# Kernel tuning notes

Measured on AMD Instinct MI355X. Metric: run time of the kernel, lower is better.

## Reference

```python
import jax, jax.numpy as jnp
import numpy as np
from jax.scipy.special import logsumexp

NUM_STATES = 16
NUM_CHAINS = 8
NUM_NODES = 1500
NUM_ITERS = 500


def setup_inputs() -> dict:
    key = jax.random.key(0)
    k1, k2, k3, k4 = jax.random.split(key, 4)
    return {
        "unnormalized_state_init": jax.random.normal(k1, (NUM_STATES, NUM_CHAINS), jnp.float32),
        "unnormalized_chain_weights": jax.random.normal(k2, (NUM_ITERS, NUM_CHAINS), jnp.float32),
        "unnormalized_emission_matrix": jax.random.normal(k3, (NUM_STATES, 1, NUM_NODES), jnp.float32),
        "unnormalized_transition_matrix": jax.random.normal(k4, (NUM_CHAINS, NUM_STATES, NUM_STATES), jnp.float32),
    }


def reference(unnormalized_state_init, unnormalized_chain_weights,
              unnormalized_emission_matrix, unnormalized_transition_matrix):
    # log_transform_params: normalize each distribution in log domain
    log_state_init = jax.nn.log_softmax(unnormalized_state_init, axis=0)          # (S,C): over states
    log_chain_weights = jax.nn.log_softmax(unnormalized_chain_weights, axis=-1)   # (T,C): over chains
    log_emission = jax.nn.log_softmax(unnormalized_emission_matrix, axis=-1)      # (S,1,N): over nodes
    log_T_ = jax.nn.log_softmax(unnormalized_transition_matrix, axis=-1)          # (C,S,S): over next state

    T = unnormalized_chain_weights.shape[0]

    # chain-marginalized transition matrix (computed as in torch forward_model; not used downstream)
    log_mean_cw = logsumexp(log_chain_weights, axis=0) - jnp.log(jnp.asarray(T, log_chain_weights.dtype))
    _log_transition_matrix = logsumexp(log_T_ + log_mean_cw[:, None, None], axis=0)

    # sequential HMM prior recursion over tiny (S,C) state via scan
    def step(h, _):
        # h: (S,C) -> h.T: (C,S); logsumexp over previous-state axis
        new = logsumexp(h.T[:, :, None] + log_T_, axis=1).T  # (S,C)
        return new, new

    h0 = log_state_init
    _, hs = jax.lax.scan(step, h0, None, length=T - 1)
    log_hidden_state_probs = jnp.concatenate([h0[None], hs], axis=0)  # (T,S,C)

    # emission broadcast: (S,1,N) + (T,S,C,1) -> (T,S,C,N), then add chain weights
    log_observed_state_probs_ = (log_emission[None]
                                 + log_hidden_state_probs[..., None]
                                 + log_chain_weights[:, None, :, None])
    # marginalize over states then chains
    log_observed_state_probs = logsumexp(log_observed_state_probs_, axis=(1, 2))  # (T,N)
    return (log_observed_state_probs, log_observed_state_probs_, log_hidden_state_probs)
```

## Files before the change

kernel.cpp:

```cpp
#include <hip/hip_runtime.h>
#include <hip/hip_bf16.h>

#define S 16
#define C 8
#define SC 128
#define TT 500
#define NN 1500
#define NF4 375
#define CHUNK 25
#define NCHUNK 20

__device__ __forceinline__ float fexp2(float x) { return exp2f(x); }
__device__ __forceinline__ float flog2(float x) { return log2f(x); }

#define L2E 1.4426950408889634f
#define LN2 0.6931471805599453f

typedef float f4v __attribute__((ext_vector_type(4)));

#define MM(dst, Asrc, Bsrc) do {                                          \
    __syncthreads();                                                      \
    {   const int c_ = tid >> 5; const int e0_ = tid & 31;                \
        for (int r_ = 0; r_ < 8; ++r_) {                                  \
            const int e_ = e0_ + (r_ << 5);                               \
            const int i_ = e_ >> 4; const int l_ = e_ & 15;               \
            float acc_ = 0.f;                                             \
            _Pragma("unroll")                                             \
            for (int s_ = 0; s_ < S; ++s_)                                \
                acc_ += Asrc[(c_ * S + i_) * S + s_] *                    \
                        Bsrc[(c_ * S + s_) * S + l_];                     \
            dst[(c_ * S + i_) * S + l_] = acc_;                          \
        } }                                                               \
} while (0)

__global__ __launch_bounds__(256) void hmm_setup(
    const float* __restrict__ usi,
    const float* __restrict__ ucw,
    const float* __restrict__ uem,
    const float* __restrict__ utm,
    float* __restrict__ ws_lcw,
    float* __restrict__ ws_pT,
    float* __restrict__ ws_q,
    float* __restrict__ ws_emlse)
{
    __shared__ float bufT[C * S * S];
    __shared__ float bufX[C * S * S];
    __shared__ float bufY[C * S * S];
    __shared__ float bufZ[C * S * S];
    __shared__ float qbuf[C * S];
    const int tid = threadIdx.x;

    for (int t = tid; t < TT; t += 256) {
        float x[C]; float m = -1e30f;
#pragma unroll
        for (int cc = 0; cc < C; ++cc) { x[cc] = ucw[t * C + cc]; m = fmaxf(m, x[cc]); }
        float acc = 0.f;
#pragma unroll
        for (int cc = 0; cc < C; ++cc) acc += fexp2((x[cc] - m) * L2E);
        const float lse = m + flog2(acc) * LN2;
#pragma unroll
        for (int cc = 0; cc < C; ++cc) ws_lcw[t * C + cc] = x[cc] - lse;
    }

    {
        const int row = tid >> 4;
        const int ln  = tid & 15;
        const float* rp = uem + row * NN;
        float a = 0.f;
        for (int n = ln; n < NN; n += 16) a += fexp2(rp[n] * L2E);
#pragma unroll
        for (int off = 8; off >= 1; off >>= 1) a += __shfl_xor(a, off);
        if (ln == 0) ws_emlse[row] = flog2(a) * LN2;
    }

    if (tid < SC) {
        float x[S]; float m = -1e30f;
#pragma unroll
        for (int k = 0; k < S; ++k) { x[k] = utm[tid * S + k]; m = fmaxf(m, x[k]); }
        float acc = 0.f; float e[S];
#pragma unroll
        for (int k = 0; k < S; ++k) { e[k] = fexp2((x[k] - m) * L2E); acc += e[k]; }
        const float inv = 1.f / acc;
#pragma unroll
        for (int k = 0; k < S; ++k) {
            const float v = e[k] * inv;
            bufT[tid * S + k] = v;
            ws_pT[tid * S + k] = v;
        }
    }

    if (tid < C) {
        const int cc = tid;
        float x[S]; float m = -1e30f;
#pragma unroll
        for (int s0 = 0; s0 < S; ++s0) { x[s0] = usi[s0 * C + cc]; m = fmaxf(m, x[s0]); }
        float acc = 0.f; float e[S];
#pragma unroll
        for (int s0 = 0; s0 < S; ++s0) { e[s0] = fexp2((x[s0] - m) * L2E); acc += e[s0]; }
        const float inv = 1.f / acc;
#pragma unroll
        for (int s0 = 0; s0 < S; ++s0) {
            const float v = e[s0] * inv;
            qbuf[cc * S + s0] = v;
            ws_q[cc * S + s0] = v;
        }
    }

    MM(bufX, bufT, bufT);
    MM(bufY, bufX, bufX);
    MM(bufZ, bufY, bufY);
    MM(bufX, bufZ, bufZ);
    MM(bufY, bufX, bufZ);
    MM(bufX, bufY, bufT);
    __syncthreads();

    const int c5 = tid >> 4;
    const int l5 = tid & 15;
    float Acol[S];
    if (tid < 128) {
#pragma unroll
        for (int s0 = 0; s0 < S; ++s0) Acol[s0] = bufX[(c5 * S + s0) * S + l5];
    }
    for (int k = 1; k < NCHUNK; ++k) {
        float acc = 0.f;
        if (tid < 128) {
#pragma unroll
            for (int s0 = 0; s0 < S; ++s0) acc += qbuf[c5 * S + s0] * Acol[s0];
        }
        __syncthreads();
        if (tid < 128) {
            qbuf[c5 * S + l5] = acc;
            ws_q[k * SC + c5 * S + l5] = acc;
        }
        __syncthreads();
    }
}

__global__ __launch_bounds__(512) void fused_bcast(
    const float* __restrict__ uem,
    const float* __restrict__ ws_lcw,
    const float* __restrict__ ws_pT,
    const float* __restrict__ ws_q,
    const float* __restrict__ ws_emlse,
    float* __restrict__ out1,
    float* __restrict__ out2,
    float* __restrict__ out3)
{
    const int t = blockIdx.x;
    const int tid = threadIdx.x;
    __shared__ float hc[SC];
    __shared__ float Ws[S];
    __shared__ float em[S];

    if (tid >= 64 && tid < 64 + S) em[tid - 64] = ws_emlse[tid - 64];

    if (tid < 64) {
        const int c = tid >> 3;
        const int j = tid & 7;
        float Ta[S], Tb[S];
#pragma unroll
        for (int s0 = 0; s0 < S; ++s0) {
            Ta[s0] = ws_pT[(c * S + s0) * S + j];
            Tb[s0] = ws_pT[(c * S + s0) * S + j + 8];
        }
        const int k = t / CHUNK;
        const int m = t - k * CHUNK;
        float pa = ws_q[k * SC + c * S + j];
        float pb = ws_q[k * SC + c * S + j + 8];
        const int base = c << 3;
        for (int i = 0; i < m; ++i) {
            float pv[S];
#pragma unroll
            for (int q = 0; q < 8; ++q) {
                pv[q]     = __shfl(pa, base + q);
                pv[q + 8] = __shfl(pb, base + q);
            }
            float a0 = 0.f, a1 = 0.f, a2 = 0.f, a3 = 0.f;
            float b0 = 0.f, b1 = 0.f, b2 = 0.f, b3 = 0.f;
#pragma unroll
            for (int s0 = 0; s0 < S; s0 += 4) {
                a0 = fmaf(pv[s0],     Ta[s0],     a0);
                a1 = fmaf(pv[s0 + 1], Ta[s0 + 1], a1);
                a2 = fmaf(pv[s0 + 2], Ta[s0 + 2], a2);
                a3 = fmaf(pv[s0 + 3], Ta[s0 + 3], a3);
                b0 = fmaf(pv[s0],     Tb[s0],     b0);
                b1 = fmaf(pv[s0 + 1], Tb[s0 + 1], b1);
                b2 = fmaf(pv[s0 + 2], Tb[s0 + 2], b2);
                b3 = fmaf(pv[s0 + 3], Tb[s0 + 3], b3);
            }
            pa = (a0 + a1) + (a2 + a3);
            pb = (b0 + b1) + (b2 + b3);
        }
        const float la = flog2(pa) * LN2;
        const float lb = flog2(pb) * LN2;
        out3[(size_t)t * SC + j * C + c]       = la;
        out3[(size_t)t * SC + (j + 8) * C + c] = lb;
        const float w = ws_lcw[t * C + c];
        hc[j * C + c]       = la + w;
        hc[(j + 8) * C + c] = lb + w;
    }
    __syncthreads();
    if (tid < S) {
        float mx = -1e30f;
#pragma unroll
        for (int cc = 0; cc < C; ++cc) mx = fmaxf(mx, hc[tid * C + cc]);
        float acc = 0.f;
#pragma unroll
        for (int cc = 0; cc < C; ++cc) acc += fexp2((hc[tid * C + cc] - mx) * L2E);
        Ws[tid] = mx + flog2(acc) * LN2;
    }
    __syncthreads();

    if (tid < NF4) {
        f4v acc1 = {0.f, 0.f, 0.f, 0.f};
        float* o2t = out2 + (size_t)t * SC * NN + tid * 4;
        for (int s0 = 0; s0 < S; ++s0) {
            f4v e = *(const f4v*)(uem + s0 * NN + tid * 4);
            const float el = em[s0];
            e -= el;
            const float w = Ws[s0];
            acc1.x += fexp2((e.x + w) * L2E);
            acc1.y += fexp2((e.y + w) * L2E);
            acc1.z += fexp2((e.z + w) * L2E);
            acc1.w += fexp2((e.w + w) * L2E);
            float* orow = o2t + (size_t)s0 * C * NN;
#pragma unroll
            for (int cc = 0; cc < C; ++cc) {
                const float hv = hc[s0 * C + cc];
                f4v v = e + hv;
                __builtin_nontemporal_store(v, (f4v*)(orow + (size_t)cc * NN));
            }
        }
        f4v r;
        r.x = flog2(acc1.x) * LN2;
        r.y = flog2(acc1.y) * LN2;
        r.z = flog2(acc1.z) * LN2;
        r.w = flog2(acc1.w) * LN2;
        *(f4v*)(out1 + (size_t)t * NN + tid * 4) = r;
    }
}

extern "C" void kernel_launch(void* const* d_in, const int* in_sizes, int n_in,
                              void* d_out, int out_size, void* d_ws, size_t ws_size,
                              hipStream_t stream)
{
    const float* usi = (const float*)d_in[0];
    const float* ucw = (const float*)d_in[1];
    const float* uem = (const float*)d_in[2];
    const float* utm = (const float*)d_in[3];

    float* out  = (float*)d_out;
    float* out1 = out;
    float* out2 = out + 750000;
    float* out3 = out + 750000 + 96000000;

    float* ws       = (float*)d_ws;
    float* ws_lcw   = ws;
    float* ws_pT    = ws + 4000;
    float* ws_q     = ws + 6048;
    float* ws_emlse = ws + 8608;

    hmm_setup<<<1, 256, 0, stream>>>(usi, ucw, uem, utm, ws_lcw, ws_pT, ws_q, ws_emlse);
    fused_bcast<<<TT, 512, 0, stream>>>(uem, ws_lcw, ws_pT, ws_q, ws_emlse,
                                        out1, out2, out3);
}
```

Baseline: 139.6 us.

## Move HMM recursion into single setup block and split broadcast into separate kernels

The hidden-state recursion moves out of every broadcast block and into one 1024-thread setup kernel, where 16 wavefronts each run a 32-step chunk from precomputed T^32 powers. That kernel also writes out3 and a per-(t,s) chain-weighted log term. The old fused broadcast kernel is split into an out1 kernel, which computes the reduction in the probability domain as exp(em)*g, and a streaming out2 kernel over a (16,500) grid that uses regular instead of nontemporal stores. This removes the redundant per-block sequential recursion (up to 24 steps per block) and gives the big store more, smaller blocks. The cost is an extra launch, a serial single-block setup phase, and a second read of uem.

New measurement: 172.5 us. 1.24x slower.

```diff
diff --git a/kernel.cpp b/kernel.cpp
--- a/kernel.cpp
+++ b/kernel.cpp
@@ -7,8 +7,8 @@
 #define TT 500
 #define NN 1500
 #define NF4 375
-#define CHUNK 25
-#define NCHUNK 20
+#define CHUNK 32
+#define NCHUNK 16
 
 __device__ __forceinline__ float fexp2(float x) { return exp2f(x); }
 __device__ __forceinline__ float flog2(float x) { return log2f(x); }
@@ -20,37 +20,40 @@
 
 #define MM(dst, Asrc, Bsrc) do {                                          \
     __syncthreads();                                                      \
-    {   const int c_ = tid >> 5; const int e0_ = tid & 31;                \
-        for (int r_ = 0; r_ < 8; ++r_) {                                  \
-            const int e_ = e0_ + (r_ << 5);                               \
-            const int i_ = e_ >> 4; const int l_ = e_ & 15;               \
-            float acc_ = 0.f;                                             \
-            _Pragma("unroll")                                             \
-            for (int s_ = 0; s_ < S; ++s_)                                \
-                acc_ += Asrc[(c_ * S + i_) * S + s_] *                    \
-                        Bsrc[(c_ * S + s_) * S + l_];                     \
-            dst[(c_ * S + i_) * S + l_] = acc_;                          \
-        } }                                                               \
+    for (int e_ = tid; e_ < 2048; e_ += 1024) {                           \
+        const int c_ = e_ >> 8;                                           \
+        const int i_ = (e_ >> 4) & 15;                                    \
+        const int l_ = e_ & 15;                                           \
+        float acc_ = 0.f;                                                 \
+        _Pragma("unroll")                                                 \
+        for (int s_ = 0; s_ < S; ++s_)                                    \
+            acc_ += Asrc[(c_ * S + i_) * S + s_] *                        \
+                    Bsrc[(c_ * S + s_) * S + l_];                         \
+        dst[(c_ * S + i_) * S + l_] = acc_;                              \
+    }                                                                     \
 } while (0)
 
-__global__ __launch_bounds__(256) void hmm_setup(
+__global__ __launch_bounds__(1024) void setup_all(
     const float* __restrict__ usi,
     const float* __restrict__ ucw,
     const float* __restrict__ uem,
     const float* __restrict__ utm,
     float* __restrict__ ws_lcw,
-    float* __restrict__ ws_pT,
-    float* __restrict__ ws_q,
-    float* __restrict__ ws_emlse)
+    float* __restrict__ ws_Ws,
+    float* __restrict__ ws_emlse,
+    float* __restrict__ out3)
 {
     __shared__ float bufT[C * S * S];
     __shared__ float bufX[C * S * S];
     __shared__ float bufY[C * S * S];
     __shared__ float bufZ[C * S * S];
-    __shared__ float qbuf[C * S];
+    __shared__ float qall[NCHUNK * SC];
+    __shared__ float qbuf[SC];
+    __shared__ float lcwS[TT * C];
+    __shared__ float cwpS[TT * C];
     const int tid = threadIdx.x;
 
-    for (int t = tid; t < TT; t += 256) {
+    for (int t = tid; t < TT; t += 1024) {
         float x[C]; float m = -1e30f;
 #pragma unroll
         for (int cc = 0; cc < C; ++cc) { x[cc] = ucw[t * C + cc]; m = fmaxf(m, x[cc]); }
@@ -59,10 +62,15 @@
         for (int cc = 0; cc < C; ++cc) acc += fexp2((x[cc] - m) * L2E);
         const float lse = m + flog2(acc) * LN2;
 #pragma unroll
-        for (int cc = 0; cc < C; ++cc) ws_lcw[t * C + cc] = x[cc] - lse;
-    }
-
-    {
+        for (int cc = 0; cc < C; ++cc) {
+            const float v = x[cc] - lse;
+            lcwS[t * C + cc] = v;
+            ws_lcw[t * C + cc] = v;
+            cwpS[t * C + cc] = fexp2(v * L2E);
+        }
+    }
+
+    if (tid < 256) {
         const int row = tid >> 4;
         const int ln  = tid & 15;
         const float* rp = uem + row * NN;
@@ -82,11 +90,7 @@
         for (int k = 0; k < S; ++k) { e[k] = fexp2((x[k] - m) * L2E); acc += e[k]; }
         const float inv = 1.f / acc;
 #pragma unroll
-        for (int k = 0; k < S; ++k) {
-            const float v = e[k] * inv;
-            bufT[tid * S + k] = v;
-            ws_pT[tid * S + k] = v;
-        }
+        for (int k = 0; k < S; ++k) bufT[tid * S + k] = e[k] * inv;
     }
 
     if (tid < C) {
@@ -102,7 +106,7 @@
         for (int s0 = 0; s0 < S; ++s0) {
             const float v = e[s0] * inv;
             qbuf[cc * S + s0] = v;
-            ws_q[cc * S + s0] = v;
+            qall[cc * S + s0] = v;
         }
     }
 
@@ -110,133 +114,141 @@
     MM(bufY, bufX, bufX);
     MM(bufZ, bufY, bufY);
     MM(bufX, bufZ, bufZ);
-    MM(bufY, bufX, bufZ);
-    MM(bufX, bufY, bufT);
+    MM(bufY, bufX, bufX);
     __syncthreads();
 
     const int c5 = tid >> 4;
     const int l5 = tid & 15;
     float Acol[S];
-    if (tid < 128) {
-#pragma unroll
-        for (int s0 = 0; s0 < S; ++s0) Acol[s0] = bufX[(c5 * S + s0) * S + l5];
+    if (tid < SC) {
+#pragma unroll
+        for (int s0 = 0; s0 < S; ++s0) Acol[s0] = bufY[(c5 * S + s0) * S + l5];
     }
     for (int k = 1; k < NCHUNK; ++k) {
         float acc = 0.f;
-        if (tid < 128) {
+        if (tid < SC) {
 #pragma unroll
             for (int s0 = 0; s0 < S; ++s0) acc += qbuf[c5 * S + s0] * Acol[s0];
         }
         __syncthreads();
-        if (tid < 128) {
+        if (tid < SC) {
             qbuf[c5 * S + l5] = acc;
-            ws_q[k * SC + c5 * S + l5] = acc;
+            qall[k * SC + c5 * S + l5] = acc;
         }
         __syncthreads();
     }
-}
-
-__global__ __launch_bounds__(512) void fused_bcast(
-    const float* __restrict__ uem,
-    const float* __restrict__ ws_lcw,
-    const float* __restrict__ ws_pT,
-    const float* __restrict__ ws_q,
-    const float* __restrict__ ws_emlse,
-    float* __restrict__ out1,
-    float* __restrict__ out2,
-    float* __restrict__ out3)
-{
-    const int t = blockIdx.x;
-    const int tid = threadIdx.x;
-    __shared__ float hc[SC];
-    __shared__ float Ws[S];
-    __shared__ float em[S];
-
-    if (tid >= 64 && tid < 64 + S) em[tid - 64] = ws_emlse[tid - 64];
-
-    if (tid < 64) {
-        const int c = tid >> 3;
-        const int j = tid & 7;
-        float Ta[S], Tb[S];
-#pragma unroll
-        for (int s0 = 0; s0 < S; ++s0) {
-            Ta[s0] = ws_pT[(c * S + s0) * S + j];
-            Tb[s0] = ws_pT[(c * S + s0) * S + j + 8];
-        }
-        const int k = t / CHUNK;
-        const int m = t - k * CHUNK;
-        float pa = ws_q[k * SC + c * S + j];
-        float pb = ws_q[k * SC + c * S + j + 8];
-        const int base = c << 3;
-        for (int i = 0; i < m; ++i) {
-            float pv[S];
-#pragma unroll
-            for (int q = 0; q < 8; ++q) {
-                pv[q]     = __shfl(pa, base + q);
-                pv[q + 8] = __shfl(pb, base + q);
-            }
-            float a0 = 0.f, a1 = 0.f, a2 = 0.f, a3 = 0.f;
-            float b0 = 0.f, b1 = 0.f, b2 = 0.f, b3 = 0.f;
-#pragma unroll
-            for (int s0 = 0; s0 < S; s0 += 4) {
-                a0 = fmaf(pv[s0],     Ta[s0],     a0);
-                a1 = fmaf(pv[s0 + 1], Ta[s0 + 1], a1);
-                a2 = fmaf(pv[s0 + 2], Ta[s0 + 2], a2);
-                a3 = fmaf(pv[s0 + 3], Ta[s0 + 3], a3);
-                b0 = fmaf(pv[s0],     Tb[s0],     b0);
-                b1 = fmaf(pv[s0 + 1], Tb[s0 + 1], b1);
-                b2 = fmaf(pv[s0 + 2], Tb[s0 + 2], b2);
-                b3 = fmaf(pv[s0 + 3], Tb[s0 + 3], b3);
-            }
-            pa = (a0 + a1) + (a2 + a3);
-            pb = (b0 + b1) + (b2 + b3);
-        }
+
+    const int w = tid >> 6;
+    const int lane = tid & 63;
+    const int c = lane >> 3;
+    const int j = lane & 7;
+    float Ta[S], Tb[S];
+#pragma unroll
+    for (int s0 = 0; s0 < S; ++s0) {
+        Ta[s0] = bufT[(c * S + s0) * S + j];
+        Tb[s0] = bufT[(c * S + s0) * S + j + 8];
+    }
+    float pa = qall[w * SC + c * S + j];
+    float pb = qall[w * SC + c * S + j + 8];
+    const int base = c << 3;
+
+    for (int i = 0; i < CHUNK; ++i) {
+        const int t = w * CHUNK + i;
+        if (t >= TT) break;
         const float la = flog2(pa) * LN2;
         const float lb = flog2(pb) * LN2;
         out3[(size_t)t * SC + j * C + c]       = la;
         out3[(size_t)t * SC + (j + 8) * C + c] = lb;
-        const float w = ws_lcw[t * C + c];
-        hc[j * C + c]       = la + w;
-        hc[(j + 8) * C + c] = lb + w;
-    }
+        const float cw = cwpS[t * C + c];
+        float ea = pa * cw, eb = pb * cw;
+        ea += __shfl_xor(ea, 8); ea += __shfl_xor(ea, 16); ea += __shfl_xor(ea, 32);
+        eb += __shfl_xor(eb, 8); eb += __shfl_xor(eb, 16); eb += __shfl_xor(eb, 32);
+        if (c == 0) {
+            ws_Ws[t * S + j]     = flog2(ea) * LN2;
+            ws_Ws[t * S + j + 8] = flog2(eb) * LN2;
+        }
+        float pv[S];
+#pragma unroll
+        for (int q = 0; q < 8; ++q) {
+            pv[q]     = __shfl(pa, base + q);
+            pv[q + 8] = __shfl(pb, base + q);
+        }
+        float a0 = 0.f, a1 = 0.f, a2 = 0.f, a3 = 0.f;
+        float b0 = 0.f, b1 = 0.f, b2 = 0.f, b3 = 0.f;
+#pragma unroll
+        for (int s0 = 0; s0 < S; s0 += 4) {
+            a0 = fmaf(pv[s0],     Ta[s0],     a0);
+            a1 = fmaf(pv[s0 + 1], Ta[s0 + 1], a1);
+            a2 = fmaf(pv[s0 + 2], Ta[s0 + 2], a2);
+            a3 = fmaf(pv[s0 + 3], Ta[s0 + 3], a3);
+            b0 = fmaf(pv[s0],     Tb[s0],     b0);
+            b1 = fmaf(pv[s0 + 1], Tb[s0 + 1], b1);
+            b2 = fmaf(pv[s0 + 2], Tb[s0 + 2], b2);
+            b3 = fmaf(pv[s0 + 3], Tb[s0 + 3], b3);
+        }
+        pa = (a0 + a1) + (a2 + a3);
+        pb = (b0 + b1) + (b2 + b3);
+    }
+}
+
+__global__ __launch_bounds__(256) void out1_kernel(
+    const float* __restrict__ uem,
+    const float* __restrict__ ws_Ws,
+    const float* __restrict__ ws_emlse,
+    float* __restrict__ out1)
+{
+    const int t = blockIdx.x;
+    const int tid = threadIdx.x;
+    __shared__ float g[S];
+    if (tid < S) g[tid] = fexp2((ws_Ws[t * S + tid] - ws_emlse[tid]) * L2E);
     __syncthreads();
-    if (tid < S) {
-        float mx = -1e30f;
-#pragma unroll
-        for (int cc = 0; cc < C; ++cc) mx = fmaxf(mx, hc[tid * C + cc]);
-        float acc = 0.f;
-#pragma unroll
-        for (int cc = 0; cc < C; ++cc) acc += fexp2((hc[tid * C + cc] - mx) * L2E);
-        Ws[tid] = mx + flog2(acc) * LN2;
-    }
+
+    for (int idx = tid; idx < NF4; idx += 256) {
+        f4v acc = {0.f, 0.f, 0.f, 0.f};
+#pragma unroll
+        for (int s0 = 0; s0 < S; ++s0) {
+            const f4v e = *(const f4v*)(uem + s0 * NN + idx * 4);
+            const float gs = g[s0];
+            acc.x += fexp2(e.x * L2E) * gs;
+            acc.y += fexp2(e.y * L2E) * gs;
+            acc.z += fexp2(e.z * L2E) * gs;
+            acc.w += fexp2(e.w * L2E) * gs;
+        }
+        f4v r;
+        r.x = flog2(acc.x) * LN2;
+        r.y = flog2(acc.y) * LN2;
+        r.z = flog2(acc.z) * LN2;
+        r.w = flog2(acc.w) * LN2;
+        *(f4v*)(out1 + (size_t)t * NN + idx * 4) = r;
+    }
+}
+
+__global__ __launch_bounds__(256) void stream_kernel(
+    const float* __restrict__ uem,
+    const float* __restrict__ out3,
+    const float* __restrict__ ws_lcw,
+    const float* __restrict__ ws_emlse,
+    float* __restrict__ out2)
+{
+    const int s0 = blockIdx.x;
+    const int t  = blockIdx.y;
+    const int tid = threadIdx.x;
+    __shared__ float hcv[C];
+    __shared__ float emv;
+    if (tid < C) hcv[tid] = out3[(size_t)t * SC + s0 * C + tid] + ws_lcw[t * C + tid];
+    if (tid == C) emv = ws_emlse[s0];
     __syncthreads();
-
-    if (tid < NF4) {
-        f4v acc1 = {0.f, 0.f, 0.f, 0.f};
-        float* o2t = out2 + (size_t)t * SC * NN + tid * 4;
-        for (int s0 = 0; s0 < S; ++s0) {
-            f4v e = *(const f4v*)(uem + s0 * NN + tid * 4);
-            const float el = em[s0];
-            e -= el;
-            const float w = Ws[s0];
-            acc1.x += fexp2((e.x + w) * L2E);
-            acc1.y += fexp2((e.y + w) * L2E);
-            acc1.z += fexp2((e.z + w) * L2E);
-            acc1.w += fexp2((e.w + w) * L2E);
-            float* orow = o2t + (size_t)s0 * C * NN;
-#pragma unroll
-            for (int cc = 0; cc < C; ++cc) {
-                const float hv = hc[s0 * C + cc];
-                f4v v = e + hv;
-                __builtin_nontemporal_store(v, (f4v*)(orow + (size_t)cc * NN));
-            }
-        }
-        f4v r;
-        r.x = flog2(acc1.x) * LN2;
-        r.y = flog2(acc1.y) * LN2;
-        r.z = flog2(acc1.z) * LN2;
-        r.w = flog2(acc1.w) * LN2;
-        *(f4v*)(out1 + (size_t)t * NN + tid * 4) = r;
+    const float el = emv;
+
+    float* o2 = out2 + (size_t)t * SC * NN + (size_t)s0 * C * NN;
+    for (int idx = tid; idx < NF4; idx += 256) {
+        f4v e = *(const f4v*)(uem + s0 * NN + idx * 4);
+        e -= el;
+        float* o = o2 + idx * 4;
+#pragma unroll
+        for (int cc = 0; cc < C; ++cc) {
+            *(f4v*)(o + (size_t)cc * NN) = e + hcv[cc];
+        }
     }
 }
 
@@ -256,11 +268,11 @@
 
     float* ws       = (float*)d_ws;
     float* ws_lcw   = ws;
-    float* ws_pT    = ws + 4000;
-    float* ws_q     = ws + 6048;
-    float* ws_emlse = ws + 8608;
-
-    hmm_setup<<<1, 256, 0, stream>>>(usi, ucw, uem, utm, ws_lcw, ws_pT, ws_q, ws_emlse);
-    fused_bcast<<<TT, 512, 0, stream>>>(uem, ws_lcw, ws_pT, ws_q, ws_emlse,
-                                        out1, out2, out3);
-}
+    float* ws_Ws    = ws + 4000;
+    float* ws_emlse = ws + 12000;
+
+    setup_all<<<1, 1024, 0, stream>>>(usi, ucw, uem, utm,
+                                      ws_lcw, ws_Ws, ws_emlse, out3);
+    out1_kernel<<<TT, 256, 0, stream>>>(uem, ws_Ws, ws_emlse, out1);
+    stream_kernel<<<dim3(S, TT), 256, 0, stream>>>(uem, out3, ws_lcw, ws_emlse, out2);
+}
```

## Split fused broadcast into chunked recursion, row-streaming writer, and probability-domain out1 kernel

Applied to the files above, without the earlier changes.

Replaces the single per-timestep fused kernel with three kernels. A 20-block kernel runs each 25-step chunk of the recursion once instead of recomputing prefixes per timestep, writes out3, and emits per-state mixture weights in the probability domain. A 2000-block streaming kernel writes the large out2 tensor row by row with plain stores. A separate out1 kernel computes the logsumexp as a weighted sum of exp(emission). This removes redundant serial recursion work and spreads the 384MB write across more blocks, at the cost of extra launches and of out1 losing max-subtraction, which risks underflow or overflow.

Measured after the change: 132.2 us. 1.06x faster.

```diff
diff --git a/kernel.cpp b/kernel.cpp
--- a/kernel.cpp
+++ b/kernel.cpp
@@ -39,6 +39,7 @@
     const float* __restrict__ uem,
     const float* __restrict__ utm,
     float* __restrict__ ws_lcw,
+    float* __restrict__ ws_cwp,
     float* __restrict__ ws_pT,
     float* __restrict__ ws_q,
     float* __restrict__ ws_emlse)
@@ -59,7 +60,11 @@
         for (int cc = 0; cc < C; ++cc) acc += fexp2((x[cc] - m) * L2E);
         const float lse = m + flog2(acc) * LN2;
 #pragma unroll
-        for (int cc = 0; cc < C; ++cc) ws_lcw[t * C + cc] = x[cc] - lse;
+        for (int cc = 0; cc < C; ++cc) {
+            const float v = x[cc] - lse;
+            ws_lcw[t * C + cc] = v;
+            ws_cwp[t * C + cc] = fexp2(v * L2E);
+        }
     }
 
     {
@@ -136,107 +141,133 @@
     }
 }
 
-__global__ __launch_bounds__(512) void fused_bcast(
-    const float* __restrict__ uem,
-    const float* __restrict__ ws_lcw,
+__global__ __launch_bounds__(64) void hmm_chunks(
     const float* __restrict__ ws_pT,
     const float* __restrict__ ws_q,
+    const float* __restrict__ ws_cwp,
     const float* __restrict__ ws_emlse,
-    float* __restrict__ out1,
-    float* __restrict__ out2,
-    float* __restrict__ out3)
-{
-    const int t = blockIdx.x;
-    const int tid = threadIdx.x;
-    __shared__ float hc[SC];
-    __shared__ float Ws[S];
-    __shared__ float em[S];
-
-    if (tid >= 64 && tid < 64 + S) em[tid - 64] = ws_emlse[tid - 64];
-
-    if (tid < 64) {
-        const int c = tid >> 3;
-        const int j = tid & 7;
-        float Ta[S], Tb[S];
-#pragma unroll
-        for (int s0 = 0; s0 < S; ++s0) {
-            Ta[s0] = ws_pT[(c * S + s0) * S + j];
-            Tb[s0] = ws_pT[(c * S + s0) * S + j + 8];
-        }
-        const int k = t / CHUNK;
-        const int m = t - k * CHUNK;
-        float pa = ws_q[k * SC + c * S + j];
-        float pb = ws_q[k * SC + c * S + j + 8];
-        const int base = c << 3;
-        for (int i = 0; i < m; ++i) {
-            float pv[S];
-#pragma unroll
-            for (int q = 0; q < 8; ++q) {
-                pv[q]     = __shfl(pa, base + q);
-                pv[q + 8] = __shfl(pb, base + q);
-            }
-            float a0 = 0.f, a1 = 0.f, a2 = 0.f, a3 = 0.f;
-            float b0 = 0.f, b1 = 0.f, b2 = 0.f, b3 = 0.f;
-#pragma unroll
-            for (int s0 = 0; s0 < S; s0 += 4) {
-                a0 = fmaf(pv[s0],     Ta[s0],     a0);
-                a1 = fmaf(pv[s0 + 1], Ta[s0 + 1], a1);
-                a2 = fmaf(pv[s0 + 2], Ta[s0 + 2], a2);
-                a3 = fmaf(pv[s0 + 3], Ta[s0 + 3], a3);
-                b0 = fmaf(pv[s0],     Tb[s0],     b0);
-                b1 = fmaf(pv[s0 + 1], Tb[s0 + 1], b1);
-                b2 = fmaf(pv[s0 + 2], Tb[s0 + 2], b2);
-                b3 = fmaf(pv[s0 + 3], Tb[s0 + 3], b3);
-            }
-            pa = (a0 + a1) + (a2 + a3);
-            pb = (b0 + b1) + (b2 + b3);
-        }
+    float* __restrict__ out3,
+    float* __restrict__ ws_gval)
+{
+    const int k = blockIdx.x;
+    const int lane = threadIdx.x;
+    const int c = lane >> 3;
+    const int j = lane & 7;
+
+    float Ta[S], Tb[S];
+#pragma unroll
+    for (int s0 = 0; s0 < S; ++s0) {
+        Ta[s0] = ws_pT[(c * S + s0) * S + j];
+        Tb[s0] = ws_pT[(c * S + s0) * S + j + 8];
+    }
+    float pa = ws_q[k * SC + c * S + j];
+    float pb = ws_q[k * SC + c * S + j + 8];
+    const float invEa = fexp2(-ws_emlse[j] * L2E);
+    const float invEb = fexp2(-ws_emlse[j + 8] * L2E);
+
+    const int base = c << 3;
+    for (int i = 0; i < CHUNK; ++i) {
+        const int t = k * CHUNK + i;
         const float la = flog2(pa) * LN2;
         const float lb = flog2(pb) * LN2;
         out3[(size_t)t * SC + j * C + c]       = la;
         out3[(size_t)t * SC + (j + 8) * C + c] = lb;
-        const float w = ws_lcw[t * C + c];
-        hc[j * C + c]       = la + w;
-        hc[(j + 8) * C + c] = lb + w;
-    }
+
+        const float cw = ws_cwp[t * C + c];
+        float ea = pa * cw, eb = pb * cw;
+        ea += __shfl_xor(ea, 8); ea += __shfl_xor(ea, 16); ea += __shfl_xor(ea, 32);
+        eb += __shfl_xor(eb, 8); eb += __shfl_xor(eb, 16); eb += __shfl_xor(eb, 32);
+        if (lane < 8) {
+            ws_gval[t * S + lane]     = ea * invEa;
+            ws_gval[t * S + lane + 8] = eb * invEb;
+        }
+        if (i == CHUNK - 1) break;
+
+        float pv[S];
+#pragma unroll
+        for (int q = 0; q < 8; ++q) {
+            pv[q]     = __shfl(pa, base + q);
+            pv[q + 8] = __shfl(pb, base + q);
+        }
+        float a0 = 0.f, a1 = 0.f, a2 = 0.f, a3 = 0.f;
+        float b0 = 0.f, b1 = 0.f, b2 = 0.f, b3 = 0.f;
+#pragma unroll
+        for (int s0 = 0; s0 < S; s0 += 4) {
+            a0 = fmaf(pv[s0],     Ta[s0],     a0);
+            a1 = fmaf(pv[s0 + 1], Ta[s0 + 1], a1);
+            a2 = fmaf(pv[s0 + 2], Ta[s0 + 2], a2);
+            a3 = fmaf(pv[s0 + 3], Ta[s0 + 3], a3);
+            b0 = fmaf(pv[s0],     Tb[s0],     b0);
+            b1 = fmaf(pv[s0 + 1], Tb[s0 + 1], b1);
+            b2 = fmaf(pv[s0 + 2], Tb[s0 + 2], b2);
+            b3 = fmaf(pv[s0 + 3], Tb[s0 + 3], b3);
+        }
+        pa = (a0 + a1) + (a2 + a3);
+        pb = (b0 + b1) + (b2 + b3);
+    }
+}
+
+__global__ __launch_bounds__(256) void stream_kernel(
+    const float* __restrict__ uem,
+    const float* __restrict__ out3,
+    const float* __restrict__ ws_lcw,
+    const float* __restrict__ ws_emlse,
+    float* __restrict__ out2)
+{
+    const int tid = threadIdx.x;
+    const int row0 = blockIdx.x << 5;
+    float* outp = out2 + (size_t)row0 * NN;
+
+    for (int rr = 0; rr < 16; ++rr) {
+        const int r0 = row0 + rr * 2;
+        const int t  = r0 >> 7;
+        const int s  = (r0 >> 3) & 15;
+        const int c0 = r0 & 7;
+        const float el = ws_emlse[s];
+        const float av0 = out3[r0]     + ws_lcw[t * C + c0]     - el;
+        const float av1 = out3[r0 + 1] + ws_lcw[t * C + c0 + 1] - el;
+        const float* rowp = uem + s * NN;
+        float* po = outp + (size_t)rr * 2 * NN;
+#pragma unroll
+        for (int off = tid; off < 750; off += 256) {
+            const bool hi = off >= NF4;
+            const float a = hi ? av1 : av0;
+            const int o = hi ? off - NF4 : off;
+            f4v e = *(const f4v*)(rowp + o * 4);
+            e += a;
+            *(f4v*)(po + (size_t)off * 4) = e;
+        }
+    }
+}
+
+__global__ __launch_bounds__(256) void out1_kernel(
+    const float* __restrict__ uem,
+    const float* __restrict__ ws_gval,
+    float* __restrict__ out1)
+{
+    const int t = blockIdx.x;
+    const int tid = threadIdx.x;
+    __shared__ float g[S];
+    if (tid < S) g[tid] = ws_gval[t * S + tid];
     __syncthreads();
-    if (tid < S) {
-        float mx = -1e30f;
-#pragma unroll
-        for (int cc = 0; cc < C; ++cc) mx = fmaxf(mx, hc[tid * C + cc]);
-        float acc = 0.f;
-#pragma unroll
-        for (int cc = 0; cc < C; ++cc) acc += fexp2((hc[tid * C + cc] - mx) * L2E);
-        Ws[tid] = mx + flog2(acc) * LN2;
-    }
-    __syncthreads();
-
-    if (tid < NF4) {
-        f4v acc1 = {0.f, 0.f, 0.f, 0.f};
-        float* o2t = out2 + (size_t)t * SC * NN + tid * 4;
+
+    for (int idx = tid; idx < NF4; idx += 256) {
+        f4v acc = {0.f, 0.f, 0.f, 0.f};
+#pragma unroll
         for (int s0 = 0; s0 < S; ++s0) {
-            f4v e = *(const f4v*)(uem + s0 * NN + tid * 4);
-            const float el = em[s0];
-            e -= el;
-            const float w = Ws[s0];
-            acc1.x += fexp2((e.x + w) * L2E);
-            acc1.y += fexp2((e.y + w) * L2E);
-            acc1.z += fexp2((e.z + w) * L2E);
-            acc1.w += fexp2((e.w + w) * L2E);
-            float* orow = o2t + (size_t)s0 * C * NN;
-#pragma unroll
-            for (int cc = 0; cc < C; ++cc) {
-                const float hv = hc[s0 * C + cc];
-                f4v v = e + hv;
-                __builtin_nontemporal_store(v, (f4v*)(orow + (size_t)cc * NN));
-            }
+            const f4v e = *(const f4v*)(uem + s0 * NN + idx * 4);
+            const float gs = g[s0];
+            acc.x += fexp2(e.x * L2E) * gs;
+            acc.y += fexp2(e.y * L2E) * gs;
+            acc.z += fexp2(e.z * L2E) * gs;
+            acc.w += fexp2(e.w * L2E) * gs;
         }
         f4v r;
-        r.x = flog2(acc1.x) * LN2;
-        r.y = flog2(acc1.y) * LN2;
-        r.z = flog2(acc1.z) * LN2;
-        r.w = flog2(acc1.w) * LN2;
-        *(f4v*)(out1 + (size_t)t * NN + tid * 4) = r;
+        r.x = flog2(acc.x) * LN2;
+        r.y = flog2(acc.y) * LN2;
+        r.z = flog2(acc.z) * LN2;
+        r.w = flog2(acc.w) * LN2;
+        *(f4v*)(out1 + (size_t)t * NN + idx * 4) = r;
     }
 }
 
@@ -256,11 +287,16 @@
 
     float* ws       = (float*)d_ws;
     float* ws_lcw   = ws;
-    float* ws_pT    = ws + 4000;
-    float* ws_q     = ws + 6048;
-    float* ws_emlse = ws + 8608;
-
-    hmm_setup<<<1, 256, 0, stream>>>(usi, ucw, uem, utm, ws_lcw, ws_pT, ws_q, ws_emlse);
-    fused_bcast<<<TT, 512, 0, stream>>>(uem, ws_lcw, ws_pT, ws_q, ws_emlse,
-                                        out1, out2, out3);
-}
+    float* ws_cwp   = ws + 4000;
+    float* ws_pT    = ws + 8000;
+    float* ws_q     = ws + 10048;
+    float* ws_emlse = ws + 12608;
+    float* ws_gval  = ws + 12624;
+
+    hmm_setup<<<1, 256, 0, stream>>>(usi, ucw, uem, utm,
+                                     ws_lcw, ws_cwp, ws_pT, ws_q, ws_emlse);
+    hmm_chunks<<<NCHUNK, 64, 0, stream>>>(ws_pT, ws_q, ws_cwp, ws_emlse,
+                                          out3, ws_gval);
+    stream_kernel<<<2000, 256, 0, stream>>>(uem, out3, ws_lcw, ws_emlse, out2);
+    out1_kernel<<<TT, 256, 0, stream>>>(uem, ws_gval, out1);
+}
```
